# Kernel optimization log

Hardware: AMD Instinct MI355X
Metric: run time of the kernel (lower is better)

Reference implementation:

```python
import jax, jax.numpy as jnp
import numpy as np

SERIALIZATION_FACTOR = 4

def setup_inputs() -> dict:
    key = jax.random.key(0)
    k1, k2 = jax.random.split(key)
    indices = jax.random.randint(k1, (8, 2048), 0, 50304, dtype=jnp.int64)
    weight = jax.random.normal(k2, (50304, 1024), dtype=jnp.float32)
    return {"indices": indices, "weight": weight}

def reference(indices, weight):
    num_embeddings, _ = weight.shape
    split_size = num_embeddings // SERIALIZATION_FACTOR
    x_sum = None
    for i in range(SERIALIZATION_FACTOR):
        split_indices = indices - i * split_size
        mask = (split_indices >= 0) & (split_indices < split_size)
        split_indices = split_indices * mask  # clamp out-of-range to 0 within split
        # gather from the i-th table shard: [B, S, D]
        x = weight[i * split_size:(i + 1) * split_size][split_indices]
        x = x * mask[..., None].astype(x.dtype)
        x_sum = x if x_sum is None else x_sum + x
    return x_sum
```

## Files before the change

### kernel.cpp

```cpp
#include <hip/hip_runtime.h>
#include <hip/hip_bf16.h>


#define EMB_DIM 1024
#define VEC_PER_ROW (EMB_DIM / 4)

__global__ __launch_bounds__(256) void SerializedEmbedding_7121055777167_kernel(
    const int* __restrict__ indices,
    const float* __restrict__ weight,
    float* __restrict__ out,
    int num_tokens)
{
    const int token = blockIdx.x;
    if (token >= num_tokens) return;

    const int row = indices[token];

    const float4* __restrict__ src =
        reinterpret_cast<const float4*>(weight + (size_t)row * EMB_DIM);
    float4* __restrict__ dst =
        reinterpret_cast<float4*>(out + (size_t)token * EMB_DIM);

    dst[threadIdx.x] = src[threadIdx.x];
}

extern "C" void kernel_launch(void* const* d_in, const int* in_sizes, int n_in,
                              void* d_out, int out_size, void* d_ws, size_t ws_size,
                              hipStream_t stream)
{
    const int*   indices = (const int*)d_in[0];
    const float* weight  = (const float*)d_in[1];
    float*       out     = (float*)d_out;

    const int num_tokens = in_sizes[0];

    dim3 grid(num_tokens);
    dim3 block(VEC_PER_ROW);

    SerializedEmbedding_7121055777167_kernel<<<grid, block, 0, stream>>>(
        indices, weight, out, num_tokens);
}
```

Before: 269.7 us.

## Gather four rows per wave with batched loads and nontemporal stores

Restructures the embedding gather so each 64-lane wave handles four tokens, loading the four indices as one vector and issuing all sixteen 16-byte row loads before any stores. Output writes use nontemporal stores to avoid polluting cache with streamed output. This raises memory-level parallelism per thread and cuts the block count, at the cost of more registers per thread and a scalar tail path. The vectorized index load assumes 16-byte alignment of indices at multiples of four tokens.

```diff
diff --git a/kernel.cpp b/kernel.cpp
--- a/kernel.cpp
+++ b/kernel.cpp
@@ -1,27 +1,67 @@
 #include <hip/hip_runtime.h>
-#include <hip/hip_bf16.h>
 
 
 #define EMB_DIM 1024
-#define VEC_PER_ROW (EMB_DIM / 4)
+#define F4_PER_ROW (EMB_DIM / 4)
+#define TOKENS_PER_WAVE 4
+#define WAVES_PER_BLOCK 4
+#define BLOCK_THREADS 256
+#define TOKENS_PER_BLOCK (TOKENS_PER_WAVE * WAVES_PER_BLOCK)
 
-__global__ __launch_bounds__(256) void SerializedEmbedding_7121055777167_kernel(
+typedef float f32x4 __attribute__((ext_vector_type(4)));
+typedef int   i32x4 __attribute__((ext_vector_type(4)));
+
+__global__ __launch_bounds__(BLOCK_THREADS) void SerializedEmbedding_7121055777167_kernel(
     const int* __restrict__ indices,
     const float* __restrict__ weight,
     float* __restrict__ out,
     int num_tokens)
 {
-    const int token = blockIdx.x;
-    if (token >= num_tokens) return;
+    const int wave = threadIdx.x >> 6;
+    const int lane = threadIdx.x & 63;
 
-    const int row = indices[token];
+    const int t0 = (blockIdx.x * WAVES_PER_BLOCK + wave) * TOKENS_PER_WAVE;
+    if (t0 >= num_tokens) return;
 
-    const float4* __restrict__ src =
-        reinterpret_cast<const float4*>(weight + (size_t)row * EMB_DIM);
-    float4* __restrict__ dst =
-        reinterpret_cast<float4*>(out + (size_t)token * EMB_DIM);
+    const f32x4* __restrict__ w4 = reinterpret_cast<const f32x4*>(weight);
+    f32x4* __restrict__ o4       = reinterpret_cast<f32x4*>(out);
 
-    dst[threadIdx.x] = src[threadIdx.x];
+    if (t0 + TOKENS_PER_WAVE <= num_tokens) {
+        const i32x4 idx4 = *reinterpret_cast<const i32x4*>(indices + t0);
+
+        const size_t r0 = (size_t)idx4.x * F4_PER_ROW;
+        const size_t r1 = (size_t)idx4.y * F4_PER_ROW;
+        const size_t r2 = (size_t)idx4.z * F4_PER_ROW;
+        const size_t r3 = (size_t)idx4.w * F4_PER_ROW;
+
+        f32x4 v[TOKENS_PER_WAVE][4];
+        #pragma unroll
+        for (int k = 0; k < 4; ++k) {
+            v[0][k] = w4[r0 + lane + k * 64];
+            v[1][k] = w4[r1 + lane + k * 64];
+            v[2][k] = w4[r2 + lane + k * 64];
+            v[3][k] = w4[r3 + lane + k * 64];
+        }
+
+        #pragma unroll
+        for (int t = 0; t < TOKENS_PER_WAVE; ++t) {
+            const size_t ob = (size_t)(t0 + t) * F4_PER_ROW;
+            #pragma unroll
+            for (int k = 0; k < 4; ++k) {
+                __builtin_nontemporal_store(v[t][k], &o4[ob + lane + k * 64]);
+            }
+        }
+    } else {
+        for (int t = t0; t < num_tokens; ++t) {
+            const size_t rb = (size_t)indices[t] * F4_PER_ROW;
+            const size_t ob = (size_t)t * F4_PER_ROW;
+            #pragma unroll
+            for (int k = 0; k < 4; ++k) {
+                __builtin_nontemporal_store(w4[rb + lane + k * 64],
+                                            &o4[ob + lane + k * 64]);
+            }
+        }
+    }
 }
 
 extern "C" void kernel_launch(void* const* d_in, const int* in_sizes, int n_in,
@@ -34,9 +74,8 @@
 
     const int num_tokens = in_sizes[0];
 
-    dim3 grid(num_tokens);
-    dim3 block(VEC_PER_ROW);
+    const int grid = (num_tokens + TOKENS_PER_BLOCK - 1) / TOKENS_PER_BLOCK;
 
-    SerializedEmbedding_7121055777167_kernel<<<grid, block, 0, stream>>>(
+    SerializedEmbedding_7121055777167_kernel<<<dim3(grid), dim3(BLOCK_THREADS), 0, stream>>>(
         indices, weight, out, num_tokens);
 }
```

Result: no change. 270.5 us (+0.3%).
